# Kernel optimization log

Hardware: AMD Instinct MI355X
Metric: run time of the kernel (lower is better)

## Reference

```python
import jax, jax.numpy as jnp
import numpy as np

N_SUBJECTS = 64
N_LABELS = 16
DENS_TEMP = 0.1  # args.ProtoSim_dens_temp


def setup_inputs() -> dict:
    key = jax.random.key(0)
    k1, k2, k3 = jax.random.split(key, 3)
    B, V, D = 16384, 2, 512
    X_data = jax.random.normal(k1, (B, V, D), dtype=jnp.float32)
    subject = jax.random.randint(k2, (B,), 0, N_SUBJECTS)
    labels = jax.random.randint(k3, (B,), 0, N_LABELS)
    return {"X_data": X_data, "subject": subject, "labels": labels}


def reference(X_data, subject, labels):
    B, V, D = X_data.shape  # V == contrast_count == 2 (code doubles subject/labels once)
    K = N_SUBJECTS * N_LABELS
    # torch.cat(torch.unbind(X, dim=1), dim=0) -> [V*B, D]
    cf = jnp.transpose(X_data, (1, 0, 2)).reshape(V * B, D)
    subj2 = jnp.concatenate([subject, subject])
    lab2 = jnp.concatenate([labels, labels])
    # group id: groups enumerated sorted-by-(subject,label), i.e. g = s*C + l
    gid = subj2 * N_LABELS + lab2
    ones = jnp.ones((V * B,), dtype=cf.dtype)
    counts = jax.ops.segment_sum(ones, gid, num_segments=K)  # [K]
    safe_cnt = jnp.maximum(counts, 1.0)
    centroid = jax.ops.segment_sum(cf, gid, num_segments=K) / safe_cnt[:, None]  # [K, D]
    # per-sample euclidean distance to own group centroid (torch.cdist)
    dist = jnp.linalg.norm(cf - centroid[gid], axis=1)  # [V*B]
    # density_g = mean(sqrt(dist)) / log(n_g + 10) for n_g > 1, else dmax; then clip & scale
    mean_sqrt = jax.ops.segment_sum(jnp.sqrt(dist), gid, num_segments=K) / safe_cnt
    density = mean_sqrt / jnp.log(counts + 10.0)
    density = jnp.where(counts > 1, density, 0.0)
    density = jnp.where(counts > 1, density, density.max())
    density = jnp.clip(density, jnp.percentile(density, 10), jnp.percentile(density, 90))
    density = DENS_TEMP * density / density.mean()
    density = jax.lax.stop_gradient(density)  # torch builds it via .tolist()/numpy
    # mask: different subject AND same label vs each group prototype
    g_subj = jnp.arange(K) // N_LABELS
    g_lab = jnp.arange(K) % N_LABELS
    mask = ((subj2[:, None] != g_subj[None, :]) & (lab2[:, None] == g_lab[None, :])).astype(cf.dtype)  # [V*B, K]
    # with N_SUBJECTS > 1 every row has >= 1 positive group -> no rows deleted
    sim = jnp.matmul(cf, centroid.T) / density[None, :]  # [V*B, K]
    sim = sim - jax.lax.stop_gradient(jnp.max(sim, axis=1, keepdims=True))
    positive_sim = sim * mask
    # CrossEntropyLoss(reduction='none') with soft (unnormalized) targets = mask
    logp = jax.nn.log_softmax(positive_sim, axis=1)
    loss_per_row = -(mask * logp).sum(axis=1) / mask.sum(axis=1)
    return loss_per_row.mean()
```

## Files before the change

### kernel.cpp

```cpp
#include <hip/hip_runtime.h>


typedef __bf16 v8bf __attribute__((ext_vector_type(8)));
typedef __bf16 v4bf __attribute__((ext_vector_type(4)));
typedef float  v4f  __attribute__((ext_vector_type(4)));
typedef float  v16f __attribute__((ext_vector_type(16)));
typedef unsigned int u32x4 __attribute__((ext_vector_type(4)));

#define B_ROWS 16384
#define ROWS   32768
#define NGRP   1024
#define DIM    512
#define LOG2E  1.4426950408889634f
#define LN2    0.6931471805599453f

__device__ __forceinline__ float wredSum(float v){
#pragma unroll
  for (int o = 32; o > 0; o >>= 1) v += __shfl_xor(v, o);
  return v;
}
__device__ __forceinline__ float wredMax(float v){
#pragma unroll
  for (int o = 32; o > 0; o >>= 1) v = fmaxf(v, __shfl_xor(v, o));
  return v;
}

__device__ __forceinline__ void gload16(const void* g, void* lds){
  __builtin_amdgcn_global_load_lds(
      (const __attribute__((address_space(1))) void*)g,
      (__attribute__((address_space(3))) void*)lds, 16, 0, 0);
}

__global__ void kA2(const int* __restrict__ subj, const int* __restrict__ lab,
                    int* __restrict__ base_cnt, int* __restrict__ gid_arr){
  int i = blockIdx.x * 256 + threadIdx.x;
  int g = subj[i] * 16 + lab[i];
  gid_arr[i] = g;
  atomicAdd(&base_cnt[g], 1);
}

__global__ void kA3(const int* __restrict__ base_cnt, int* __restrict__ offs,
                    int* __restrict__ fillp){
  __shared__ int sb[NGRP];
  int t = threadIdx.x;
  int c = base_cnt[t];
  sb[t] = c;
  __syncthreads();
  for (int off = 1; off < NGRP; off <<= 1){
    int v = (t >= off) ? sb[t - off] : 0;
    __syncthreads();
    sb[t] += v;
    __syncthreads();
  }
  int ex = sb[t] - c;
  offs[t] = ex;
  fillp[t] = ex;
}

__global__ void kA4(const int* __restrict__ gid_arr, int* __restrict__ fillp,
                    int* __restrict__ row_list){
  int i = blockIdx.x * 256 + threadIdx.x;
  int pos = atomicAdd(&fillp[gid_arr[i]], 1);
  row_list[pos] = i;
}

__global__ void kB(const float* __restrict__ X, const int* __restrict__ base_cnt,
                   const int* __restrict__ offs, const int* __restrict__ row_list,
                   float* __restrict__ cent_f, __bf16* __restrict__ cent_b){
  int g = blockIdx.x, t = threadIdx.x;
  int n = base_cnt[g], off = offs[g];
  float ax = 0.f, ay = 0.f, az = 0.f, aw = 0.f;
  for (int j = 0; j < n; ++j){
    int r = row_list[off + j];
    const float4* p = (const float4*)(X + (size_t)r * 1024);
    float4 a = p[t];
    float4 b = p[t + 128];
    ax += a.x + b.x; ay += a.y + b.y; az += a.z + b.z; aw += a.w + b.w;
  }
  int cnt2 = 2 * n;
  float inv = 1.0f / (float)(cnt2 > 1 ? cnt2 : 1);
  float4 c; c.x = ax * inv; c.y = ay * inv; c.z = az * inv; c.w = aw * inv;
  ((float4*)(cent_f + (size_t)g * DIM))[t] = c;
  v4bf cb; cb[0] = (__bf16)c.x; cb[1] = (__bf16)c.y; cb[2] = (__bf16)c.z; cb[3] = (__bf16)c.w;
  *(v4bf*)(cent_b + (size_t)g * DIM + t * 4) = cb;
}

__global__ void kC(const float* __restrict__ X, const int* __restrict__ subj,
                   const int* __restrict__ lab, const float* __restrict__ cent_f,
                   float* __restrict__ msq, __bf16* __restrict__ cfb){
  int w = threadIdx.x >> 6, lane = threadIdx.x & 63;
  int r = blockIdx.x * 4 + w;
  int i = r & (B_ROWS - 1), v = r >> 14;
  int g = subj[i] * 16 + lab[i];
  const float4* xr = (const float4*)(X + ((size_t)(i * 2 + v)) * DIM);
  const float4* cr = (const float4*)(cent_f + (size_t)g * DIM);
  float4 x0 = xr[lane], x1 = xr[lane + 64];
  float4 c0 = cr[lane], c1 = cr[lane + 64];
  float s = 0.f, d;
  d = x0.x - c0.x; s += d * d;  d = x0.y - c0.y; s += d * d;
  d = x0.z - c0.z; s += d * d;  d = x0.w - c0.w; s += d * d;
  d = x1.x - c1.x; s += d * d;  d = x1.y - c1.y; s += d * d;
  d = x1.z - c1.z; s += d * d;  d = x1.w - c1.w; s += d * d;
  v4bf b0; b0[0]=(__bf16)x0.x; b0[1]=(__bf16)x0.y; b0[2]=(__bf16)x0.z; b0[3]=(__bf16)x0.w;
  v4bf b1; b1[0]=(__bf16)x1.x; b1[1]=(__bf16)x1.y; b1[2]=(__bf16)x1.z; b1[3]=(__bf16)x1.w;
  *(v4bf*)(cfb + (size_t)r * DIM + lane * 4)       = b0;
  *(v4bf*)(cfb + (size_t)r * DIM + 256 + lane * 4) = b1;
  s = wredSum(s);
  if (lane == 0){
    float dist = sqrtf(s);
    atomicAdd(&msq[g], sqrtf(dist));
  }
}

__global__ void kD(const int* __restrict__ base_cnt, const float* __restrict__ msq,
                   float* __restrict__ scale2){
  __shared__ float sd[NGRP];
  __shared__ float ss[NGRP];
  __shared__ float rb[16];
  int t = threadIdx.x;
  int lane = t & 63, wid = t >> 6;
  int cnt2 = 2 * base_cnt[t];
  float safe = (float)(cnt2 > 1 ? cnt2 : 1);
  float v = (msq[t] / safe) / logf((float)cnt2 + 10.0f);
  float d1 = (cnt2 > 1) ? v : 0.0f;
  float wm = wredMax(d1);
  if (lane == 0) rb[wid] = wm;
  __syncthreads();
  float x = (lane < 16) ? rb[lane] : -3.0e38f;
  if (wid == 0){ x = wredMax(x); if (lane == 0) rb[0] = x; }
  __syncthreads();
  float dmax = rb[0];
  float d2 = (cnt2 > 1) ? d1 : dmax;
  sd[t] = d2;
  __syncthreads();
  int rank = 0;
  for (int j = 0; j < NGRP; ++j){
    float dj = sd[j];
    rank += (dj < d2) || (dj == d2 && j < t);
  }
  ss[rank] = d2;
  __syncthreads();
  float p10 = ss[102] + 0.3f * (ss[103] - ss[102]);
  float p90 = ss[920] + 0.7f * (ss[921] - ss[920]);
  float c = fminf(fmaxf(d2, p10), p90);
  __syncthreads();
  float wsm = wredSum(c);
  if (lane == 0) rb[wid] = wsm;
  __syncthreads();
  float y = (lane < 16) ? rb[lane] : 0.0f;
  if (wid == 0){ y = wredSum(y); if (lane == 0) rb[0] = y; }
  __syncthreads();
  float mean = rb[0] * (1.0f / 1024.0f);
  scale2[t] = LOG2E * mean / (0.1f * c);
}

__global__ __launch_bounds__(256, 1)
void kE(const __bf16* __restrict__ cfb, const __bf16* __restrict__ centb,
        const float* __restrict__ scale2, const int* __restrict__ gid_arr,
        float* __restrict__ out){
  __shared__ u32x4 tile[2][2048];
  __shared__ float sscale[NGRP];
  __shared__ float redM[128], redE[128], redS[128];
  int tid = threadIdx.x, lane = tid & 63;
  int w = tid >> 6, rw = w & 1, h = w >> 1;
  int l31 = lane & 31, lhi = lane >> 5;
  int row = blockIdx.x * 64 + rw * 32 + l31;

  ((v4f*)sscale)[tid] = ((const v4f*)scale2)[tid];

  u32x4 breg[32];
  {
    const u32x4* rp = (const u32x4*)cfb + (size_t)row * 64 + lhi;
#pragma unroll
    for (int m = 0; m < 32; ++m) breg[m] = rp[2 * m];
  }
  int g0 = gid_arr[row & (B_ROWS - 1)];
  int rsub = g0 >> 4, rlab = g0 & 15;
  int jm = rlab & 3;
  bool qm1 = (rlab >> 3) & 1;
  bool lhi_ok = ((rlab >> 2) & 1) == lhi;

  const char* gsrc = (const char*)centb;
  auto stage = [&](int t2, int buf){
    int i2 = t2 >> 3, ks2 = t2 & 7;
#pragma unroll
    for (int it = 0; it < 8; ++it){
      int p = it * 256 + tid;
      int trow = p >> 3, clin = p & 7;
      int c = clin ^ (trow & 7);
      int grow = i2 * 128 + (trow & 127) + ((trow >> 7) << 9);
      const void* src = gsrc + ((size_t)(grow * 64 + ks2 * 8 + c) << 4);
      void* dst = (void*)&tile[buf][it * 256 + (w << 6)];
      gload16(src, dst);
    }
  };

  float M = -3.0e38f, E = 0.f, S = 0.f;
  stage(0, 0);
  asm volatile("s_waitcnt vmcnt(0) lgkmcnt(0)" ::: "memory");
  __builtin_amdgcn_sched_barrier(0);
  __builtin_amdgcn_s_barrier();
  __builtin_amdgcn_sched_barrier(0);

  for (int i = 0; i < 4; ++i){
    v16f acc[4];
#pragma unroll
    for (int fm = 0; fm < 4; ++fm)
#pragma unroll
      for (int e = 0; e < 16; ++e) acc[fm][e] = 0.f;

#pragma unroll
    for (int ks = 0; ks < 8; ++ks){
      int t2 = i * 8 + ks;
      int buf = t2 & 1;
      if (t2 < 31){
        stage(t2 + 1, buf ^ 1);
        asm volatile("s_waitcnt vmcnt(8)" ::: "memory");
      } else {
        asm volatile("s_waitcnt vmcnt(0)" ::: "memory");
      }
      __builtin_amdgcn_sched_barrier(0);
      __builtin_amdgcn_s_barrier();
      __builtin_amdgcn_sched_barrier(0);
#pragma unroll
      for (int kk = 0; kk < 4; ++kk){
#pragma unroll
        for (int fm = 0; fm < 4; ++fm){
          int tr = h * 128 + fm * 32 + l31;
          u32x4 af = tile[buf][tr * 8 + ((kk * 2 + lhi) ^ (tr & 7))];
          acc[fm] = __builtin_amdgcn_mfma_f32_32x32x16_bf16(
              __builtin_bit_cast(v8bf, af),
              __builtin_bit_cast(v8bf, breg[ks * 4 + kk]),
              acc[fm], 0, 0, 0);
        }
      }
      __builtin_amdgcn_sched_barrier(0);
      __builtin_amdgcn_s_barrier();
      __builtin_amdgcn_sched_barrier(0);
    }

    float mloc = -3.0e38f;
#pragma unroll
    for (int fm = 0; fm < 4; ++fm){
      int sbase = h * 512 + i * 128 + fm * 32 + lhi * 4;
#pragma unroll
      for (int q = 0; q < 4; ++q){
        v4f sc = *(const v4f*)&sscale[sbase + q * 8];
#pragma unroll
        for (int j = 0; j < 4; ++j){
          float vv = acc[fm][q * 4 + j] * sc[j];
          acc[fm][q * 4 + j] = vv;
          mloc = fmaxf(mloc, vv);
        }
      }
    }
    float Mn = fmaxf(M, mloc);
    float eadd = 0.f, sadd = 0.f;
#pragma unroll
    for (int fm = 0; fm < 4; ++fm){
      float t0 = (jm == 0) ? acc[fm][0]  : (jm == 1) ? acc[fm][1]  : (jm == 2) ? acc[fm][2]  : acc[fm][3];
      float t1 = (jm == 0) ? acc[fm][4]  : (jm == 1) ? acc[fm][5]  : (jm == 2) ? acc[fm][6]  : acc[fm][7];
      float t2s= (jm == 0) ? acc[fm][8]  : (jm == 1) ? acc[fm][9]  : (jm == 2) ? acc[fm][10] : acc[fm][11];
      float t3 = (jm == 0) ? acc[fm][12] : (jm == 1) ? acc[fm][13] : (jm == 2) ? acc[fm][14] : acc[fm][15];
      float u0 = qm1 ? t1 : t0;
      float u1 = qm1 ? t3 : t2s;
      int gs = h * 32 + i * 8 + fm * 2;
      float m0 = (lhi_ok && (gs     != rsub)) ? 1.0f : 0.0f;
      float m1 = (lhi_ok && (gs + 1 != rsub)) ? 1.0f : 0.0f;
      eadd += m0 * exp2f(u0 - Mn) + m1 * exp2f(u1 - Mn);
      sadd += m0 * u0 + m1 * u1;
    }
    E = E * exp2f(M - Mn) + eadd;
    S += sadd;
    M = Mn;
  }

  {
    float mo = __shfl_xor(M, 32), eo = __shfl_xor(E, 32), so = __shfl_xor(S, 32);
    float mn = fmaxf(M, mo);
    E = E * exp2f(M - mn) + eo * exp2f(mo - mn);
    S += so; M = mn;
  }
  if (lhi == 0){
    redM[w * 32 + l31] = M; redE[w * 32 + l31] = E; redS[w * 32 + l31] = S;
  }
  __syncthreads();
  if (tid < 64){
    float m0 = redM[tid], e0 = redE[tid], s0 = redS[tid];
    float m1 = redM[tid + 64], e1 = redE[tid + 64], s1 = redS[tid + 64];
    float mn = fmaxf(m0, m1);
    float Ee = e0 * exp2f(m0 - mn) + e1 * exp2f(m1 - mn);
    float Ss = s0 + s1;
    float loss = logf(961.0f + Ee) + LN2 * mn - LN2 * (Ss * (1.0f / 63.0f));
    float ws = wredSum(loss);
    if (tid == 0) atomicAdd(out, ws * (1.0f / (float)ROWS));
  }
}

extern "C" void kernel_launch(void* const* d_in, const int* in_sizes, int n_in,
                              void* d_out, int out_size, void* d_ws, size_t ws_size,
                              hipStream_t stream){
  const float* X   = (const float*)d_in[0];
  const int* subj  = (const int*)d_in[1];
  const int* lab   = (const int*)d_in[2];
  char* ws = (char*)d_ws;

  int*    base_cnt = (int*)(ws + 0);
  float*  msq      = (float*)(ws + 4096);
  int*    offs     = (int*)(ws + 8192);
  int*    fillp    = (int*)(ws + 12288);
  int*    gid_arr  = (int*)(ws + 16384);
  int*    row_list = (int*)(ws + 81920);
  float*  scale2   = (float*)(ws + 147456);
  float*  cent_f   = (float*)(ws + 151552);
  __bf16* cent_b   = (__bf16*)(ws + 2248704);
  __bf16* cfb      = (__bf16*)(ws + 3297280);

  hipMemsetAsync(ws, 0, 8192, stream);
  hipMemsetAsync(d_out, 0, sizeof(float), stream);

  kA2<<<64, 256, 0, stream>>>(subj, lab, base_cnt, gid_arr);
  kA3<<<1, 1024, 0, stream>>>(base_cnt, offs, fillp);
  kA4<<<64, 256, 0, stream>>>(gid_arr, fillp, row_list);
  kB <<<NGRP, 128, 0, stream>>>(X, base_cnt, offs, row_list, cent_f, cent_b);
  kC <<<8192, 256, 0, stream>>>(X, subj, lab, cent_f, msq, cfb);
  kD <<<1, 1024, 0, stream>>>(base_cnt, msq, scale2);
  kE <<<512, 256, 0, stream>>>(cfb, cent_b, scale2, gid_arr, (float*)d_out);
}
```

Baseline: 173.1 us.

## Fuse bucketing kernels and deepen kE pipeline with larger blocks

Merges the three small bucketing kernels (count, scan, scatter) into one single-block kernel that counts and fills with LDS atomics, which removes two launches and the global atomics. kE now uses 512-thread blocks covering 128 rows, so each staged centroid tile is shared by twice as many rows. It also gets a 4-buffer LDS ring prefetching two stages ahead, which lets it drop the trailing barrier per k-step. The cost is a single-block kA that may serialize, fewer kE blocks (256) across the CUs, more LDS use per block, and correctness that depends on the 4-deep ring spacing to avoid reuse races.

```diff
diff --git a/kernel.cpp b/kernel.cpp
--- a/kernel.cpp
+++ b/kernel.cpp
@@ -31,37 +31,43 @@
       (__attribute__((address_space(3))) void*)lds, 16, 0, 0);
 }
 
-__global__ void kA2(const int* __restrict__ subj, const int* __restrict__ lab,
-                    int* __restrict__ base_cnt, int* __restrict__ gid_arr){
-  int i = blockIdx.x * 256 + threadIdx.x;
-  int g = subj[i] * 16 + lab[i];
-  gid_arr[i] = g;
-  atomicAdd(&base_cnt[g], 1);
-}
-
-__global__ void kA3(const int* __restrict__ base_cnt, int* __restrict__ offs,
-                    int* __restrict__ fillp){
-  __shared__ int sb[NGRP];
+__global__ __launch_bounds__(1024)
+void kA(const int* __restrict__ subj, const int* __restrict__ lab,
+        int* __restrict__ base_cnt, int* __restrict__ offs,
+        int* __restrict__ gid_arr, int* __restrict__ row_list){
+  __shared__ int cnt[NGRP];
+  __shared__ int fill[NGRP];
   int t = threadIdx.x;
-  int c = base_cnt[t];
-  sb[t] = c;
-  __syncthreads();
+  cnt[t] = 0;
+  __syncthreads();
+  int gl[16];
+#pragma unroll
+  for (int k = 0; k < 16; ++k){
+    int i = k * 1024 + t;
+    int g = subj[i] * 16 + lab[i];
+    gl[k] = g;
+    gid_arr[i] = g;
+    atomicAdd(&cnt[g], 1);
+  }
+  __syncthreads();
+  int c = cnt[t];
   for (int off = 1; off < NGRP; off <<= 1){
-    int v = (t >= off) ? sb[t - off] : 0;
+    int v = (t >= off) ? cnt[t - off] : 0;
     __syncthreads();
-    sb[t] += v;
+    cnt[t] += v;
     __syncthreads();
   }
-  int ex = sb[t] - c;
+  int ex = cnt[t] - c;
+  base_cnt[t] = c;
   offs[t] = ex;
-  fillp[t] = ex;
-}
-
-__global__ void kA4(const int* __restrict__ gid_arr, int* __restrict__ fillp,
-                    int* __restrict__ row_list){
-  int i = blockIdx.x * 256 + threadIdx.x;
-  int pos = atomicAdd(&fillp[gid_arr[i]], 1);
-  row_list[pos] = i;
+  fill[t] = ex;
+  __syncthreads();
+#pragma unroll
+  for (int k = 0; k < 16; ++k){
+    int i = k * 1024 + t;
+    int pos = atomicAdd(&fill[gl[k]], 1);
+    row_list[pos] = i;
+  }
 }
 
 __global__ void kB(const float* __restrict__ X, const int* __restrict__ base_cnt,
@@ -154,19 +160,19 @@
   scale2[t] = LOG2E * mean / (0.1f * c);
 }
 
-__global__ __launch_bounds__(256, 1)
+__global__ __launch_bounds__(512, 1)
 void kE(const __bf16* __restrict__ cfb, const __bf16* __restrict__ centb,
         const float* __restrict__ scale2, const int* __restrict__ gid_arr,
         float* __restrict__ out){
-  __shared__ u32x4 tile[2][2048];
+  __shared__ u32x4 tile[4][2048];
   __shared__ float sscale[NGRP];
-  __shared__ float redM[128], redE[128], redS[128];
+  __shared__ float redM[256], redE[256], redS[256];
   int tid = threadIdx.x, lane = tid & 63;
-  int w = tid >> 6, rw = w & 1, h = w >> 1;
+  int w = tid >> 6, rw = w & 3, h = w >> 2;
   int l31 = lane & 31, lhi = lane >> 5;
-  int row = blockIdx.x * 64 + rw * 32 + l31;
-
-  ((v4f*)sscale)[tid] = ((const v4f*)scale2)[tid];
+  int row = blockIdx.x * 128 + rw * 32 + l31;
+
+  if (tid < 256) ((v4f*)sscale)[tid] = ((const v4f*)scale2)[tid];
 
   u32x4 breg[32];
   {
@@ -184,24 +190,26 @@
   auto stage = [&](int t2, int buf){
     int i2 = t2 >> 3, ks2 = t2 & 7;
 #pragma unroll
-    for (int it = 0; it < 8; ++it){
-      int p = it * 256 + tid;
+    for (int it = 0; it < 4; ++it){
+      int p = it * 512 + tid;
       int trow = p >> 3, clin = p & 7;
       int c = clin ^ (trow & 7);
       int grow = i2 * 128 + (trow & 127) + ((trow >> 7) << 9);
       const void* src = gsrc + ((size_t)(grow * 64 + ks2 * 8 + c) << 4);
-      void* dst = (void*)&tile[buf][it * 256 + (w << 6)];
+      void* dst = (void*)&tile[buf][it * 512 + (w << 6)];
       gload16(src, dst);
     }
   };
 
   float M = -3.0e38f, E = 0.f, S = 0.f;
   stage(0, 0);
+  stage(1, 1);
   asm volatile("s_waitcnt vmcnt(0) lgkmcnt(0)" ::: "memory");
   __builtin_amdgcn_sched_barrier(0);
   __builtin_amdgcn_s_barrier();
   __builtin_amdgcn_sched_barrier(0);
 
+#pragma unroll
   for (int i = 0; i < 4; ++i){
     v16f acc[4];
 #pragma unroll
@@ -211,11 +219,13 @@
 
 #pragma unroll
     for (int ks = 0; ks < 8; ++ks){
-      int t2 = i * 8 + ks;
-      int buf = t2 & 1;
-      if (t2 < 31){
-        stage(t2 + 1, buf ^ 1);
+      const int t2 = i * 8 + ks;
+      const int buf = t2 & 3;
+      if (t2 <= 29){
+        stage(t2 + 2, (t2 + 2) & 3);
         asm volatile("s_waitcnt vmcnt(8)" ::: "memory");
+      } else if (t2 == 30){
+        asm volatile("s_waitcnt vmcnt(4)" ::: "memory");
       } else {
         asm volatile("s_waitcnt vmcnt(0)" ::: "memory");
       }
@@ -234,9 +244,6 @@
               acc[fm], 0, 0, 0);
         }
       }
-      __builtin_amdgcn_sched_barrier(0);
-      __builtin_amdgcn_s_barrier();
-      __builtin_amdgcn_sched_barrier(0);
     }
 
     float mloc = -3.0e38f;
@@ -285,15 +292,15 @@
     redM[w * 32 + l31] = M; redE[w * 32 + l31] = E; redS[w * 32 + l31] = S;
   }
   __syncthreads();
-  if (tid < 64){
+  if (tid < 128){
     float m0 = redM[tid], e0 = redE[tid], s0 = redS[tid];
-    float m1 = redM[tid + 64], e1 = redE[tid + 64], s1 = redS[tid + 64];
+    float m1 = redM[tid + 128], e1 = redE[tid + 128], s1 = redS[tid + 128];
     float mn = fmaxf(m0, m1);
     float Ee = e0 * exp2f(m0 - mn) + e1 * exp2f(m1 - mn);
     float Ss = s0 + s1;
     float loss = logf(961.0f + Ee) + LN2 * mn - LN2 * (Ss * (1.0f / 63.0f));
     float ws = wredSum(loss);
-    if (tid == 0) atomicAdd(out, ws * (1.0f / (float)ROWS));
+    if ((tid & 63) == 0) atomicAdd(out, ws * (1.0f / (float)ROWS));
   }
 }
 
@@ -308,22 +315,19 @@
   int*    base_cnt = (int*)(ws + 0);
   float*  msq      = (float*)(ws + 4096);
   int*    offs     = (int*)(ws + 8192);
-  int*    fillp    = (int*)(ws + 12288);
-  int*    gid_arr  = (int*)(ws + 16384);
-  int*    row_list = (int*)(ws + 81920);
-  float*  scale2   = (float*)(ws + 147456);
-  float*  cent_f   = (float*)(ws + 151552);
-  __bf16* cent_b   = (__bf16*)(ws + 2248704);
-  __bf16* cfb      = (__bf16*)(ws + 3297280);
+  int*    gid_arr  = (int*)(ws + 12288);
+  int*    row_list = (int*)(ws + 77824);
+  float*  scale2   = (float*)(ws + 143360);
+  float*  cent_f   = (float*)(ws + 147456);
+  __bf16* cent_b   = (__bf16*)(ws + 2244608);
+  __bf16* cfb      = (__bf16*)(ws + 3293184);
 
   hipMemsetAsync(ws, 0, 8192, stream);
   hipMemsetAsync(d_out, 0, sizeof(float), stream);
 
-  kA2<<<64, 256, 0, stream>>>(subj, lab, base_cnt, gid_arr);
-  kA3<<<1, 1024, 0, stream>>>(base_cnt, offs, fillp);
-  kA4<<<64, 256, 0, stream>>>(gid_arr, fillp, row_list);
+  kA <<<1, 1024, 0, stream>>>(subj, lab, base_cnt, offs, gid_arr, row_list);
   kB <<<NGRP, 128, 0, stream>>>(X, base_cnt, offs, row_list, cent_f, cent_b);
   kC <<<8192, 256, 0, stream>>>(X, subj, lab, cent_f, msq, cfb);
   kD <<<1, 1024, 0, stream>>>(base_cnt, msq, scale2);
-  kE <<<512, 256, 0, stream>>>(cfb, cent_b, scale2, gid_arr, (float*)d_out);
-}
+  kE <<<256, 512, 0, stream>>>(cfb, cent_b, scale2, gid_arr, (float*)d_out);
+}
```

After: 206.0 us. 19.0% more time.
